# Performance work log

Hardware: AMD Instinct MI355X
Metric: run time of the kernel (lower is better)

The kernel has to match this reference:

```python
import jax, jax.numpy as jnp
import numpy as np

D_MODEL = 512
STATE_DIM = 64
INNER = 768  # ceil(512 * 1.5)
KERNEL = 3
EPS = 1e-5
DELTA_MIN = 1e-4
DELTA_MAX = 3.0


def _hippo_legS(n):
    A = np.zeros((n, n), dtype=np.float32)
    for i in range(n):
        ci = np.sqrt(2 * i + 1)
        for m in range(i + 1):
            cm = np.sqrt(2 * m + 1)
            if i == m:
                A[i, m] = -(2 * i + 1)
            else:
                sign = -1.0 if (i - m) % 2 == 0 else 1.0
                A[i, m] = sign * ci * cm
    idx = np.arange(n, dtype=np.float32)
    B = np.sqrt(2.0 * idx + 1.0)
    C = B.copy()
    C[1::2] *= -1.0
    return A, B, C


def setup_inputs() -> dict:
    key = jax.random.key(0)
    k1, k2, k3, k4 = jax.random.split(key, 4)
    x = jax.random.normal(k1, (8, 2048, D_MODEL), dtype=jnp.float32)
    norm_w = jnp.ones((D_MODEL,), jnp.float32)
    norm_b = jnp.zeros((D_MODEL,), jnp.float32)
    W_in = jax.random.normal(k2, (D_MODEL, 3 * INNER), jnp.float32) * 0.02
    conv_w = jax.random.normal(k3, (INNER, KERNEL), jnp.float32) * 0.2  # torch (C,1,k) squeezed
    A_np, B_np, C_np = _hippo_legS(STATE_DIM)
    scale = 1.0 / np.sqrt(INNER)
    A = jnp.asarray(A_np)
    B_mat = jnp.asarray(np.repeat(B_np[:, None], INNER, axis=1) * scale)   # [N, inner]
    C_mat = jnp.asarray(np.repeat(C_np[None, :], INNER, axis=0) * scale)   # [inner, N]
    W_out = jax.random.normal(k4, (INNER, D_MODEL), jnp.float32) * 0.02
    return {"x": x, "norm_w": norm_w, "norm_b": norm_b, "W_in": W_in,
            "conv_w": conv_w, "A": A, "B_mat": B_mat, "C_mat": C_mat, "W_out": W_out}


def reference(x, norm_w, norm_b, W_in, conv_w, A, B_mat, C_mat, W_out):
    Bsz, L, D = x.shape
    N = A.shape[0]
    # LayerNorm (biased variance, as torch)
    mu = x.mean(-1, keepdims=True)
    var = jnp.mean((x - mu) ** 2, axis=-1, keepdims=True)
    h = (x - mu) / jnp.sqrt(var + EPS) * norm_w + norm_b
    proj = h @ W_in                                 # [B, L, 3*inner]
    data, gate, delta_raw = jnp.split(proj, 3, axis=-1)
    # causal depthwise conv: torch pads k-1 both sides then truncates to L
    k = conv_w.shape[1]
    xp = jnp.pad(data, ((0, 0), (k - 1, 0), (0, 0)))
    kern = conv_w.T[:, None, :]                     # [k, 1, inner] (WIO)
    conv = jax.lax.conv_general_dilated(
        xp, kern, window_strides=(1,), padding='VALID',
        dimension_numbers=('NWC', 'WIO', 'NWC'), feature_group_count=INNER)
    u = jax.nn.silu(conv)                           # [B, L, inner]
    delta = jnp.minimum(jax.nn.softplus(delta_raw).mean(-1) + DELTA_MIN, DELTA_MAX)  # [B, L]
    I = jnp.eye(N, dtype=x.dtype)

    def step(state, inp):
        u_t, dt = inp                               # [B, inner], [B]
        Bu = jnp.einsum('nd,bd->bn', B_mat, u_t)    # [B, N]
        rhs = state + dt[:, None] * Bu
        mat = I - dt[:, None, None] * A             # [B, N, N]
        st = jnp.linalg.solve(mat, rhs[..., None])[..., 0]
        y = jnp.einsum('dn,bn->bd', C_mat, st)      # [B, inner]
        return st, y

    state0 = jnp.zeros((Bsz, N), x.dtype)
    _, ys = jax.lax.scan(step, state0, (jnp.swapaxes(u, 0, 1), delta.T))
    selective = jnp.swapaxes(ys, 0, 1)              # [B, L, inner]
    gated = jax.nn.sigmoid(gate) * selective
    return x + gated @ W_out
```

## Files before the change

kernel.cpp:

```cpp
#include <hip/hip_runtime.h>

typedef unsigned short u16;
typedef short short8 __attribute__((ext_vector_type(8)));
typedef float f32x4 __attribute__((ext_vector_type(4)));

#define D_MODEL 512
#define INNER 768
#define N3 2304
#define LSEQ 2048
#define BATCH 8
#define MROWS 16384

constexpr size_t OFF_H     = 0;
constexpr size_t OFF_WINT  = 16777216;
constexpr size_t OFF_WOUTT = 19136512;
constexpr size_t OFF_DATA  = 19922944;
constexpr size_t OFF_GATE  = 45088768;
constexpr size_t OFF_DSUM  = 70254592;
constexpr size_t OFF_YBAR  = 70451200;
constexpr size_t WS_NEEDED = 70516736;

__device__ __forceinline__ u16 f2bf(float f) {
  unsigned u = __builtin_bit_cast(unsigned, f);
  u += 0x7fffu + ((u >> 16) & 1u);
  return (u16)(u >> 16);
}
__device__ __forceinline__ float bf2f(u16 h) {
  unsigned u = ((unsigned)h) << 16;
  return __builtin_bit_cast(float, u);
}

__device__ __forceinline__ float dpp_shr1(float x) {
  int r = __builtin_amdgcn_update_dpp(0, __builtin_bit_cast(int, x),
                                      0x138 , 0xf, 0xf, true);
  return __builtin_bit_cast(float, r);
}
__device__ __forceinline__ float dpp_ror1(float x) {
  int r = __builtin_amdgcn_update_dpp(0, __builtin_bit_cast(int, x),
                                      0x13C , 0xf, 0xf, false);
  return __builtin_bit_cast(float, r);
}

#if __has_builtin(__builtin_amdgcn_global_load_lds)
__device__ __forceinline__ void cp16(const u16* g, u16* l) {
  __builtin_amdgcn_global_load_lds(
      (const __attribute__((address_space(1))) unsigned int*)g,
      (__attribute__((address_space(3))) unsigned int*)l, 16, 0, 0);
}
#else
__device__ __forceinline__ void cp16(const u16* g, u16* l) {
  *(uint4*)l = *(const uint4*)g;
}
#endif

__global__ __launch_bounds__(256) void transp2(const float* __restrict__ Wi,
                                               u16* __restrict__ WiT,
                                               const float* __restrict__ Wo,
                                               u16* __restrict__ WoT) {
  __shared__ float tile[32][33];
  int bi = blockIdx.x;
  const float* in; u16* out; int R, C, c0, r0;
  if (bi < 1152) {
    in = Wi; out = WiT; R = D_MODEL; C = N3;
    c0 = (bi % 72) * 32; r0 = (bi / 72) * 32;
  } else {
    int bj = bi - 1152;
    in = Wo; out = WoT; R = INNER; C = D_MODEL;
    c0 = (bj & 15) * 32; r0 = (bj >> 4) * 32;
  }
  int tx = threadIdx.x, ty = threadIdx.y;
#pragma unroll
  for (int i = 0; i < 4; ++i)
    tile[ty + i * 8][tx] = in[(size_t)(r0 + ty + i * 8) * C + c0 + tx];
  __syncthreads();
#pragma unroll
  for (int i = 0; i < 4; ++i)
    out[(size_t)(c0 + ty + i * 8) * R + r0 + tx] = f2bf(tile[tx][ty + i * 8]);
}

__global__ __launch_bounds__(256) void ln_kernel(const float* __restrict__ x,
                                                 const float* __restrict__ gw,
                                                 const float* __restrict__ gb,
                                                 u16* __restrict__ h,
                                                 float* __restrict__ dSum) {
  int g = blockIdx.x * 256 + threadIdx.x;
  if (g < MROWS) dSum[g] = 0.0f;
  int row = blockIdx.x * 4 + (threadIdx.x >> 6);
  int lane = threadIdx.x & 63;
  const float* xr = x + (size_t)row * D_MODEL;
  float4 v0 = *(const float4*)(xr + lane * 4);
  float4 v1 = *(const float4*)(xr + 256 + lane * 4);
  float s  = v0.x + v0.y + v0.z + v0.w + v1.x + v1.y + v1.z + v1.w;
  float s2 = v0.x * v0.x + v0.y * v0.y + v0.z * v0.z + v0.w * v0.w +
             v1.x * v1.x + v1.y * v1.y + v1.z * v1.z + v1.w * v1.w;
#pragma unroll
  for (int m = 1; m < 64; m <<= 1) { s += __shfl_xor(s, m); s2 += __shfl_xor(s2, m); }
  float mu = s * (1.0f / 512.0f);
  float var = s2 * (1.0f / 512.0f) - mu * mu;
  float rstd = rsqrtf(var + 1e-5f);
  float4 w0 = *(const float4*)(gw + lane * 4);
  float4 w1 = *(const float4*)(gw + 256 + lane * 4);
  float4 b0 = *(const float4*)(gb + lane * 4);
  float4 b1 = *(const float4*)(gb + 256 + lane * 4);
  float y0 = (v0.x - mu) * rstd * w0.x + b0.x;
  float y1 = (v0.y - mu) * rstd * w0.y + b0.y;
  float y2 = (v0.z - mu) * rstd * w0.z + b0.z;
  float y3 = (v0.w - mu) * rstd * w0.w + b0.w;
  float y4 = (v1.x - mu) * rstd * w1.x + b1.x;
  float y5 = (v1.y - mu) * rstd * w1.y + b1.y;
  float y6 = (v1.z - mu) * rstd * w1.z + b1.z;
  float y7 = (v1.w - mu) * rstd * w1.w + b1.w;
  uint2 pa, pb;
  pa.x = (unsigned)f2bf(y0) | ((unsigned)f2bf(y1) << 16);
  pa.y = (unsigned)f2bf(y2) | ((unsigned)f2bf(y3) << 16);
  pb.x = (unsigned)f2bf(y4) | ((unsigned)f2bf(y5) << 16);
  pb.y = (unsigned)f2bf(y6) | ((unsigned)f2bf(y7) << 16);
  *(uint2*)(h + (size_t)row * D_MODEL + lane * 4) = pa;
  *(uint2*)(h + (size_t)row * D_MODEL + 256 + lane * 4) = pb;
}

template <int MODE, int CT>
__global__ __launch_bounds__(512, 2) void gemm256(
    const u16* __restrict__ A, const u16* __restrict__ BT, int K,
    u16* __restrict__ dataBuf, u16* __restrict__ gateSig, float* __restrict__ deltaSum,
    const float* __restrict__ ybarp, const float* __restrict__ xres,
    float* __restrict__ outp) {
  extern __shared__ u16 lds[];
  int bi = blockIdx.x;
  int xcd = bi & 7, s = bi >> 3;
  int m0 = (xcd * 8 + s / CT) * 256;
  int n0 = (s % CT) * 256;

  int tid = threadIdx.x;
  int lane = tid & 63, wv = tid >> 6;
  int wm = wv >> 2, wn = wv & 3;

  f32x4 acc[8][4];
#pragma unroll
  for (int i = 0; i < 8; ++i)
#pragma unroll
    for (int j = 0; j < 4; ++j) acc[i][j] = (f32x4)0.0f;

  int row0 = 2 * (tid >> 3) + ((tid >> 2) & 1);
  int gq   = ((tid & 3) ^ ((tid >> 3) & 3)) * 8;
  const u16* Ab = A + (size_t)(m0 + row0) * K + gq;
  const u16* Bb = BT + (size_t)(n0 + row0) * K + gq;
  const size_t row128 = (size_t)128 * K;
  u16* ldst = &lds[tid * 8];

  int ar = wm * 128 + (lane & 15);
  int al = ar >> 1;
  int aoff0 = al * 64 + ((((ar & 1) << 2) | ((lane >> 4) ^ (al & 3)))) * 8;
  int br = wn * 64 + (lane & 15);
  int bl = br >> 1;
  int boff0 = 8192 + bl * 64 + ((((br & 1) << 2) | ((lane >> 4) ^ (bl & 3)))) * 8;

  int nsteps = K >> 5;

#define STAGE(c, t)                                     \
  do {                                                  \
    const u16* _a = Ab + (size_t)(t) * 32;              \
    const u16* _b = Bb + (size_t)(t) * 32;              \
    u16* _d = ldst + (c) * 16384;                       \
    cp16(_a, _d);                                       \
    cp16(_a + row128, _d + 4096);                       \
    cp16(_b, _d + 8192);                                \
    cp16(_b + row128, _d + 12288);                      \
  } while (0)
#define WAITBAR(N) asm volatile("s_waitcnt vmcnt(" #N ") lgkmcnt(0)\ns_barrier" ::: "memory")

  STAGE(0, 0); STAGE(1, 1); STAGE(2, 2);
  WAITBAR(8);

  for (int t = 0; t < nsteps; ++t) {
    int c = t & 3;
    if (t + 3 < nsteps) STAGE((t + 3) & 3, t + 3);
    const u16* buf = &lds[c * 16384];
    short8 af[8], bfr[4];
#pragma unroll
    for (int mt = 0; mt < 8; ++mt)
      af[mt] = *(const short8*)(buf + aoff0 + mt * 512);
#pragma unroll
    for (int nt = 0; nt < 4; ++nt)
      bfr[nt] = *(const short8*)(buf + boff0 + nt * 512);
    __builtin_amdgcn_s_setprio(1);
#pragma unroll
    for (int mt = 0; mt < 8; ++mt)
#pragma unroll
      for (int nt = 0; nt < 4; ++nt)
        acc[mt][nt] = __builtin_amdgcn_mfma_f32_16x16x32_bf16(af[mt], bfr[nt], acc[mt][nt], 0, 0, 0);
    __builtin_amdgcn_s_setprio(0);
    if (t + 1 < nsteps) {
      if (t + 3 < nsteps)      WAITBAR(8);
      else if (t + 2 < nsteps) WAITBAR(4);
      else                     WAITBAR(0);
    }
  }
#undef STAGE
#undef WAITBAR

  if (MODE == 1) {
    int region = (n0 >= 1536) ? 2 : (n0 >= 768 ? 1 : 0);
    if (region < 2) {
      u16* dst = (region == 0) ? dataBuf : gateSig;
#pragma unroll
      for (int mt = 0; mt < 8; ++mt) {
        int rbase = m0 + wm * 128 + mt * 16 + (lane >> 4) * 4;
#pragma unroll
        for (int nt = 0; nt < 4; ++nt) {
          int col = n0 - region * 768 + wn * 64 + nt * 16 + (lane & 15);
#pragma unroll
          for (int r = 0; r < 4; ++r) {
            float val = acc[mt][nt][r];
            if (region == 1) val = 1.0f / (1.0f + __expf(-val));
            dst[(size_t)(rbase + r) * INNER + col] = f2bf(val);
          }
        }
      }
    } else {
#pragma unroll
      for (int mt = 0; mt < 8; ++mt) {
        int rbase = m0 + wm * 128 + mt * 16 + (lane >> 4) * 4;
        float sums[4] = {0.f, 0.f, 0.f, 0.f};
#pragma unroll
        for (int nt = 0; nt < 4; ++nt)
#pragma unroll
          for (int r = 0; r < 4; ++r) {
            float xv = acc[mt][nt][r];
            sums[r] += fmaxf(xv, 0.0f) + __logf(1.0f + __expf(-fabsf(xv)));
          }
#pragma unroll
        for (int r = 0; r < 4; ++r) {
          float val = sums[r];
          val += __shfl_xor(val, 1); val += __shfl_xor(val, 2);
          val += __shfl_xor(val, 4); val += __shfl_xor(val, 8);
          if ((lane & 15) == 0) atomicAdd(&deltaSum[rbase + r], val);
        }
      }
    }
  } else {
#pragma unroll
    for (int mt = 0; mt < 8; ++mt) {
      int rbase = m0 + wm * 128 + mt * 16 + (lane >> 4) * 4;
#pragma unroll
      for (int r = 0; r < 4; ++r) {
        float yr = ybarp[rbase + r] * 0.036084391824351615f;
#pragma unroll
        for (int nt = 0; nt < 4; ++nt) {
          int col = n0 + wn * 64 + nt * 16 + (lane & 15);
          size_t o = (size_t)(rbase + r) * D_MODEL + col;
          outp[o] = xres[o] + yr * acc[mt][nt][r];
        }
      }
    }
  }
}

__global__ __launch_bounds__(256) void conv_reduce(const u16* __restrict__ dataBuf,
                                                   const float* __restrict__ conv_w,
                                                   const float* __restrict__ deltaSum,
                                                   float2* __restrict__ pairsG) {
  int r = blockIdx.x;
  int b = r >> 11;
  int t = r & (LSEQ - 1);
  int tid = threadIdx.x;
  float part = 0.0f;
#pragma unroll
  for (int j = 0; j < 3; ++j) {
    int d = tid + j * 256;
    float cw0 = conv_w[d * 3 + 0], cw1 = conv_w[d * 3 + 1], cw2 = conv_w[d * 3 + 2];
    float x2 = bf2f(dataBuf[(size_t)r * INNER + d]);
    float x1 = (t >= 1) ? bf2f(dataBuf[(size_t)(r - 1) * INNER + d]) : 0.0f;
    float x0 = (t >= 2) ? bf2f(dataBuf[(size_t)(r - 2) * INNER + d]) : 0.0f;
    float c = cw0 * x0 + cw1 * x1 + cw2 * x2;
    part += c / (1.0f + __expf(-c));
  }
#pragma unroll
  for (int m = 1; m < 64; m <<= 1) part += __shfl_xor(part, m);
  __shared__ float red[4];
  if ((tid & 63) == 0) red[tid >> 6] = part;
  __syncthreads();
  if (tid == 0) {
    float tot = red[0] + red[1] + red[2] + red[3];
    float v = 0.036084391824351615f * tot;
    float dt = fminf(deltaSum[r] * (1.0f / 768.0f) + 1e-4f, 3.0f);
    pairsG[b * 2240 + 64 + t] = make_float2(dt, dt * v);
  }
  if (tid == 64 && t < 64)   pairsG[b * 2240 + t] = make_float2(0.f, 0.f);
  if (tid == 128 && t < 128) pairsG[b * 2240 + 2112 + t] = make_float2(0.f, 0.f);
}

__global__ __launch_bounds__(64) void ssm_scan(const float2* __restrict__ pairsG,
                                               float* __restrict__ ybar) {
  const int b = blockIdx.x;
  const int lane = threadIdx.x;
  const float2* pb = pairsG + b * 2240 + 64 - lane;
  float* yb = ybar + b * LSEQ;

  const float ddi = 2.0f * lane + 1.0f;
  const float cg = (lane & 1) ? -ddi : ddi;
  const bool lane0 = (lane == 0);

  float2 buf[64];
#pragma unroll
  for (int j = 0; j < 32; ++j) buf[j] = pb[j];

  float P = 0.0f;
  float Q = buf[0].y * cg;
  float Y = 0.0f;

  for (int blk = 0; blk < 33; ++blk) {
    const float2* pl = pb + blk * 64 + 32;
#pragma unroll
    for (int u = 0; u < 64; ++u) {
      const int s1 = (u + 1) & 63;
      const int sl = (u + 32) & 63;
      float dt = buf[u].x;
      float gq = buf[s1].y * cg;
      float denom = fmaf(dt, ddi, 1.0f);
      float rr = __builtin_amdgcn_rcpf(denom);
      float dm1 = denom - 1.0f;
      float Pin = dpp_shr1(P);
      float spq = Pin + Q;
      P = rr * spq;
      float t2 = fmaf(-dm1, Pin, Q);
      Q = fmaf(rr, t2, gq);
      float Pror = dpp_ror1(P);
      float Yshr = dpp_shr1(Y);
      Y = lane0 ? Pror : Yshr;
      buf[sl] = pl[u];
    }
    int t_store = blk * 64 - lane;
    if ((unsigned)t_store < (unsigned)LSEQ)
      yb[t_store] = Y;
  }
}

extern "C" void kernel_launch(void* const* d_in, const int* in_sizes, int n_in,
                              void* d_out, int out_size, void* d_ws, size_t ws_size,
                              hipStream_t stream) {
  const float* x      = (const float*)d_in[0];
  const float* norm_w = (const float*)d_in[1];
  const float* norm_b = (const float*)d_in[2];
  const float* W_in   = (const float*)d_in[3];
  const float* conv_w = (const float*)d_in[4];
  const float* W_out  = (const float*)d_in[8];
  float* out = (float*)d_out;
  if (ws_size < WS_NEEDED) return;

  char* ws = (char*)d_ws;
  u16* h        = (u16*)(ws + OFF_H);
  u16* WinT     = (u16*)(ws + OFF_WINT);
  u16* WoutT    = (u16*)(ws + OFF_WOUTT);
  u16* dataBuf  = (u16*)(ws + OFF_DATA);
  u16* gateSig  = (u16*)(ws + OFF_GATE);
  float* dSum   = (float*)(ws + OFF_DSUM);
  float* ybar   = (float*)(ws + OFF_YBAR);
  float2* pairsG = (float2*)(ws + OFF_H);

  static int attr_set = 0;
  if (!attr_set) {
    hipFuncSetAttribute(reinterpret_cast<const void*>(gemm256<1, 9>),
                        hipFuncAttributeMaxDynamicSharedMemorySize, 131072);
    hipFuncSetAttribute(reinterpret_cast<const void*>(gemm256<2, 2>),
                        hipFuncAttributeMaxDynamicSharedMemorySize, 131072);
    attr_set = 1;
  }

  transp2<<<1536, dim3(32, 8), 0, stream>>>(W_in, WinT, W_out, WoutT);
  ln_kernel<<<MROWS / 4, 256, 0, stream>>>(x, norm_w, norm_b, h, dSum);
  gemm256<1, 9><<<576, 512, 131072, stream>>>(
      h, WinT, D_MODEL, dataBuf, gateSig, dSum, nullptr, nullptr, nullptr);
  conv_reduce<<<MROWS, 256, 0, stream>>>(dataBuf, conv_w, dSum, pairsG);
  ssm_scan<<<BATCH, 64, 0, stream>>>(pairsG, ybar);
  gemm256<2, 2><<<128, 512, 131072, stream>>>(
      gateSig, WoutT, INNER, nullptr, nullptr, nullptr, ybar, x, out);
}
```

Baseline: 291.0 us.

## Split GEMM main loop into half-phases and stage epilogue stores through LDS

The GEMM inner loop is split into two halves. A and B tile prefetches are interleaved with the LDS fragment reads and MFMA bursts, separated by extra barriers, so global loads overlap compute more evenly. The epilogues now write accumulators into per-wave LDS regions with a rotated column layout. They then read them back as 16-byte vectors for coalesced global stores and residual loads, replacing scattered 2- and 4-byte stores. This adds barriers and LDS traffic per step and relies on the pipeline buffers being free after the loop.

```diff
diff --git a/kernel.cpp b/kernel.cpp
--- a/kernel.cpp
+++ b/kernel.cpp
@@ -157,65 +157,110 @@
 
   int nsteps = K >> 5;
 
-#define STAGE(c, t)                                     \
+#define STAGE_A(c, t)                                   \
   do {                                                  \
     const u16* _a = Ab + (size_t)(t) * 32;              \
-    const u16* _b = Bb + (size_t)(t) * 32;              \
     u16* _d = ldst + (c) * 16384;                       \
     cp16(_a, _d);                                       \
     cp16(_a + row128, _d + 4096);                       \
+  } while (0)
+#define STAGE_B(c, t)                                   \
+  do {                                                  \
+    const u16* _b = Bb + (size_t)(t) * 32;              \
+    u16* _d = ldst + (c) * 16384;                       \
     cp16(_b, _d + 8192);                                \
     cp16(_b + row128, _d + 12288);                      \
   } while (0)
 #define WAITBAR(N) asm volatile("s_waitcnt vmcnt(" #N ") lgkmcnt(0)\ns_barrier" ::: "memory")
-
-  STAGE(0, 0); STAGE(1, 1); STAGE(2, 2);
+#define PBAR()     asm volatile("s_barrier" ::: "memory")
+#define LGKM0()    do { asm volatile("s_waitcnt lgkmcnt(0)" ::: "memory"); \
+                        __builtin_amdgcn_sched_barrier(0); } while (0)
+
+  STAGE_A(0, 0); STAGE_B(0, 0);
+  STAGE_A(1, 1); STAGE_B(1, 1);
+  STAGE_A(2, 2); STAGE_B(2, 2);
   WAITBAR(8);
 
   for (int t = 0; t < nsteps; ++t) {
     int c = t & 3;
-    if (t + 3 < nsteps) STAGE((t + 3) & 3, t + 3);
     const u16* buf = &lds[c * 16384];
-    short8 af[8], bfr[4];
-#pragma unroll
-    for (int mt = 0; mt < 8; ++mt)
-      af[mt] = *(const short8*)(buf + aoff0 + mt * 512);
+    bool stage = (t + 3 < nsteps);
+    short8 af0[4], af1[4], bfr[4];
+
+#pragma unroll
+    for (int mt = 0; mt < 4; ++mt)
+      af0[mt] = *(const short8*)(buf + aoff0 + mt * 512);
 #pragma unroll
     for (int nt = 0; nt < 4; ++nt)
       bfr[nt] = *(const short8*)(buf + boff0 + nt * 512);
+    if (stage) STAGE_A((t + 3) & 3, t + 3);
+    PBAR();
+    LGKM0();
     __builtin_amdgcn_s_setprio(1);
 #pragma unroll
-    for (int mt = 0; mt < 8; ++mt)
+    for (int mt = 0; mt < 4; ++mt)
 #pragma unroll
       for (int nt = 0; nt < 4; ++nt)
-        acc[mt][nt] = __builtin_amdgcn_mfma_f32_16x16x32_bf16(af[mt], bfr[nt], acc[mt][nt], 0, 0, 0);
+        acc[mt][nt] = __builtin_amdgcn_mfma_f32_16x16x32_bf16(af0[mt], bfr[nt], acc[mt][nt], 0, 0, 0);
     __builtin_amdgcn_s_setprio(0);
+    PBAR();
+
+#pragma unroll
+    for (int mt = 0; mt < 4; ++mt)
+      af1[mt] = *(const short8*)(buf + aoff0 + (mt + 4) * 512);
+    if (stage) STAGE_B((t + 3) & 3, t + 3);
+    PBAR();
+    LGKM0();
+    __builtin_amdgcn_s_setprio(1);
+#pragma unroll
+    for (int mt = 0; mt < 4; ++mt)
+#pragma unroll
+      for (int nt = 0; nt < 4; ++nt)
+        acc[mt + 4][nt] = __builtin_amdgcn_mfma_f32_16x16x32_bf16(af1[mt], bfr[nt], acc[mt + 4][nt], 0, 0, 0);
+    __builtin_amdgcn_s_setprio(0);
+
     if (t + 1 < nsteps) {
       if (t + 3 < nsteps)      WAITBAR(8);
       else if (t + 2 < nsteps) WAITBAR(4);
       else                     WAITBAR(0);
     }
   }
-#undef STAGE
+#undef STAGE_A
+#undef STAGE_B
 #undef WAITBAR
+#undef PBAR
+#undef LGKM0
+
+  __syncthreads();
 
   if (MODE == 1) {
     int region = (n0 >= 1536) ? 2 : (n0 >= 768 ? 1 : 0);
     if (region < 2) {
       u16* dst = (region == 0) ? dataBuf : gateSig;
-#pragma unroll
-      for (int mt = 0; mt < 8; ++mt) {
-        int rbase = m0 + wm * 128 + mt * 16 + (lane >> 4) * 4;
+      u16* wreg = &lds[wv * 8192];
+#pragma unroll
+      for (int mt = 0; mt < 8; ++mt)
 #pragma unroll
         for (int nt = 0; nt < 4; ++nt) {
-          int col = n0 - region * 768 + wn * 64 + nt * 16 + (lane & 15);
+          int colp = (nt * 16 + lane) & 63;
 #pragma unroll
           for (int r = 0; r < 4; ++r) {
+            int rowl = mt * 16 + (lane >> 4) * 4 + r;
             float val = acc[mt][nt][r];
             if (region == 1) val = 1.0f / (1.0f + __expf(-val));
-            dst[(size_t)(rbase + r) * INNER + col] = f2bf(val);
+            wreg[rowl * 64 + colp] = f2bf(val);
           }
         }
+      asm volatile("s_waitcnt lgkmcnt(0)" ::: "memory");
+      int grow0 = m0 + wm * 128;
+      int gcol0 = n0 - region * 768 + wn * 64;
+#pragma unroll
+      for (int j = 0; j < 16; ++j) {
+        int R = j * 8 + (lane >> 3);
+        int c8 = (lane & 7) * 8;
+        int colp = (c8 + (((2 * j + (lane >> 5)) & 3) << 4)) & 63;
+        uint4 v = *(const uint4*)(wreg + R * 64 + colp);
+        *(uint4*)(dst + (size_t)(grow0 + R) * INNER + gcol0 + c8) = v;
       }
     } else {
 #pragma unroll
@@ -239,19 +284,41 @@
       }
     }
   } else {
-#pragma unroll
-    for (int mt = 0; mt < 8; ++mt) {
-      int rbase = m0 + wm * 128 + mt * 16 + (lane >> 4) * 4;
-#pragma unroll
-      for (int r = 0; r < 4; ++r) {
-        float yr = ybarp[rbase + r] * 0.036084391824351615f;
-#pragma unroll
-        for (int nt = 0; nt < 4; ++nt) {
-          int col = n0 + wn * 64 + nt * 16 + (lane & 15);
-          size_t o = (size_t)(rbase + r) * D_MODEL + col;
-          outp[o] = xres[o] + yr * acc[mt][nt][r];
+    float* wregf = (float*)lds + wv * 4096;
+    int gcol0 = n0 + wn * 64;
+#pragma unroll
+    for (int P = 0; P < 2; ++P) {
+#pragma unroll
+      for (int mt = 0; mt < 4; ++mt) {
+        int mtt = P * 4 + mt;
+        int rbase = m0 + wm * 128 + mtt * 16 + (lane >> 4) * 4;
+#pragma unroll
+        for (int r = 0; r < 4; ++r) {
+          float yr = ybarp[rbase + r] * 0.036084391824351615f;
+          int rowl = mt * 16 + (lane >> 4) * 4 + r;
+#pragma unroll
+          for (int nt = 0; nt < 4; ++nt) {
+            int colp = (nt * 16 + lane) & 63;
+            wregf[rowl * 64 + colp] = yr * acc[mtt][nt][r];
+          }
         }
       }
+      asm volatile("s_waitcnt lgkmcnt(0)" ::: "memory");
+      int growP = m0 + wm * 128 + P * 64;
+#pragma unroll
+      for (int j = 0; j < 16; ++j) {
+        int R = j * 4 + (lane >> 4);
+        int c4 = (lane & 15) * 4;
+        int colp = (c4 + ((j & 3) << 4)) & 63;
+        f32x4 v = *(const f32x4*)(wregf + R * 64 + colp);
+        size_t o = (size_t)(growP + R) * D_MODEL + gcol0 + c4;
+        float4 xv = *(const float4*)(xres + o);
+        float4 ov;
+        ov.x = xv.x + v[0]; ov.y = xv.y + v[1];
+        ov.z = xv.z + v[2]; ov.w = xv.w + v[3];
+        *(float4*)(outp + o) = ov;
+      }
+      asm volatile("s_waitcnt lgkmcnt(0)" ::: "memory");
     }
   }
 }
```

New measurement: 297.6 us. 1.02x slower.
